# Optimization experiments

Measured on AMD Instinct MI355X. Metric: run time of the kernel, lower is better.

The kernel has to match this reference:

```python
import jax, jax.numpy as jnp
import numpy as np
import math

L, D, H, HD, F, G, V, P = 15, 512, 64, 8, 2048, 128, 7, 49
B, N = 4, 256


def setup_inputs() -> dict:
    key = jax.random.key(0)
    ks = jax.random.split(key, 24)
    nrm = lambda k, shape, s=0.02: (jax.random.normal(k, shape) * s).astype(jnp.float32)
    inp = {}
    inp["atom_types"] = jax.random.randint(ks[0], (B, N), 0, V)
    inp["coords"] = jax.random.normal(ks[1], (B, N, 3)) * 3.0
    inp["pair_types"] = jax.random.randint(ks[2], (B, N, N), 0, P)
    inp["mask"] = jnp.ones((B, N), dtype=bool)
    # embeddings / pair encoding params
    inp["atom_emb"] = nrm(ks[3], (V, D), 1.0).at[0].set(0.0)  # padding_idx=0
    inp["gaussian_mu"] = jax.random.normal(ks[4], (G,))
    inp["gaussian_sigma"] = jnp.ones((G,)) * 0.1
    inp["pair_a"] = jax.random.normal(ks[5], (P,)) * 0.01
    inp["pair_b"] = jax.random.normal(ks[6], (P,)) * 0.01
    inp["pl_w"] = nrm(ks[7], (G,))
    inp["pl_b"] = jnp.zeros(())
    # stacked per-layer params (leading dim L for lax.scan)
    inp["ln1_g"] = jnp.ones((L, D)); inp["ln1_b"] = jnp.zeros((L, D))
    inp["qkv_w"] = nrm(ks[8], (L, 3 * D, D)); inp["qkv_b"] = jnp.zeros((L, 3 * D))
    inp["pp_w"] = nrm(ks[9], (L, H), 0.1); inp["pp_b"] = jnp.zeros((L, H))
    inp["out_w"] = nrm(ks[10], (L, D, D)); inp["out_b"] = jnp.zeros((L, D))
    inp["ln2_g"] = jnp.ones((L, D)); inp["ln2_b"] = jnp.zeros((L, D))
    inp["ffn_w1"] = nrm(ks[11], (L, F, D)); inp["ffn_b1"] = jnp.zeros((L, F))
    inp["ffn_w2"] = nrm(ks[12], (L, D, F)); inp["ffn_b2"] = jnp.zeros((L, D))
    # SE3 head scalar affines (Linear(1,1) twice) and energy head
    inp["se3_uw"] = jnp.array(0.5); inp["se3_ub"] = jnp.array(0.01)
    inp["se3_ww"] = jnp.array(0.5); inp["se3_wb"] = jnp.array(0.01)
    inp["en_w"] = nrm(ks[13], (D,)); inp["en_b"] = jnp.zeros(())
    return inp


def _layernorm(x, g, b):
    m = x.mean(-1, keepdims=True)
    v = ((x - m) ** 2).mean(-1, keepdims=True)
    return (x - m) / jnp.sqrt(v + 1e-5) * g + b


def reference(atom_types, coords, pair_types, mask,
              atom_emb, gaussian_mu, gaussian_sigma, pair_a, pair_b, pl_w, pl_b,
              ln1_g, ln1_b, qkv_w, qkv_b, pp_w, pp_b, out_w, out_b,
              ln2_g, ln2_b, ffn_w1, ffn_b1, ffn_w2, ffn_b2,
              se3_uw, se3_ub, se3_ww, se3_wb, en_w, en_b):
    b_, n_ = atom_types.shape
    h = atom_emb[atom_types]  # [B,N,D]

    delta = coords[:, :, None, :] - coords[:, None, :, :]  # [B,N,N,3]
    d2 = (delta ** 2).sum(-1)
    dist = jnp.sqrt(jnp.maximum(d2, 1e-12))  # safe norm (grad-safe at 0)
    dist = jnp.where(mask[:, :, None], dist, 0.0)
    da = (pair_a[pair_types] * dist + pair_b[pair_types])[..., None]  # [B,N,N,1]
    gt = jnp.exp(-(da - gaussian_mu) ** 2) / (2.0 * gaussian_sigma ** 2)
    gt = gt / (gaussian_sigma * math.sqrt(2.0 * math.pi))
    gt = gt * mask[:, :, None, None]  # [B,N,N,G]
    pair_repr = gt @ pl_w + pl_b  # [B,N,N]
    pair_mask = mask[:, :, None] & mask[:, None, :]
    pair_repr = pair_repr * pair_mask

    scale = 1.0 / math.sqrt(HD)
    row_mask = mask[:, None, :, None]  # masks query rows, per original code

    def layer(hc, p):
        (l1g, l1b, qw, qb, ppw, ppb, ow, ob, l2g, l2b, w1, b1, w2, b2) = p
        x = _layernorm(hc, l1g, l1b)
        qkv = (x @ qw.T + qb).reshape(b_, n_, 3, H, HD)
        q, k, v = qkv[:, :, 0], qkv[:, :, 1], qkv[:, :, 2]
        scores = jnp.einsum('bnhd,bmhd->bhnm', q, k) * scale
        bias = pair_repr[..., None] * ppw + ppb  # [B,N,N,H]
        scores = scores + bias.transpose(0, 3, 1, 2)
        scores = jnp.where(row_mask, scores, -1e9)
        probs = jax.nn.softmax(scores, axis=-1)
        probs = jnp.where(jnp.isnan(probs), 0.0, probs)
        attn = jnp.einsum('bhnm,bmhd->bnhd', probs, v).reshape(b_, n_, D)
        hc = hc + attn @ ow.T + ob
        x2 = _layernorm(hc, l2g, l2b)
        ffn = jax.nn.gelu(x2 @ w1.T + b1, approximate=False) @ w2.T + b2
        return hc + ffn, None

    h, _ = jax.lax.scan(layer, h, (ln1_g, ln1_b, qkv_w, qkv_b, pp_w, pp_b,
                                   out_w, out_b, ln2_g, ln2_b,
                                   ffn_w1, ffn_b1, ffn_w2, ffn_b2))

    # --- SE3 equivariant head ---
    c = jax.nn.relu(pair_repr)[..., None]  # [B,N,N,1]
    c = c * se3_uw + se3_ub
    c = c * se3_ww + se3_wb
    c = c * mask[:, :, None, None]
    update = (delta * c).sum(axis=2)  # [B,N,3]
    num_valid = mask.sum(-1).astype(coords.dtype)[:, None, None] + 1e-6
    pred_coords = coords + update / num_valid

    cls = h[:, 0, :]
    pred_energy = cls @ en_w + en_b  # [B]
    return pred_coords, pred_energy


if __name__ == '__main__':
    out = reference(**setup_inputs())
    print(out[0].shape, out[1].shape)
```

## Files before the change

### kernel.cpp

```cpp
#include <hip/hip_runtime.h>
#include <hip/hip_bf16.h>
#include <math.h>

#define LAY 15
#define DIM 512
#define NH 64
#define HD 8
#define FF 2048
#define NG 128
#define BATCH 4
#define NTOK 256
#define PSTRIDE 524288

typedef __attribute__((ext_vector_type(8))) short short8;
typedef __attribute__((ext_vector_type(4))) short short4v;
typedef __attribute__((ext_vector_type(2))) short short2v;
typedef __attribute__((ext_vector_type(8))) __bf16 bf16x8;
typedef __attribute__((ext_vector_type(4))) float f32x4;

__device__ inline short f2bs(float f) {
  __bf16 b = (__bf16)f;
  return __builtin_bit_cast(short, b);
}

__global__ __launch_bounds__(256) void embed_kernel(
    const int* __restrict__ types, const float* __restrict__ emb,
    float* __restrict__ h)
{
  int idx = blockIdx.x * 256 + threadIdx.x;
  int token = idx >> 9;
  int d = idx & 511;
  h[idx] = emb[types[token] * DIM + d];
}

__global__ __launch_bounds__(256) void cvt_kernel(
    const float* __restrict__ qkvw, const float* __restrict__ outw,
    const float* __restrict__ w1, const float* __restrict__ w2,
    short* __restrict__ dst)
{
  int i = blockIdx.x * 256 + threadIdx.x;
  const float* src; int off;
  if (i < 2949120)      { src = qkvw; off = i; }
  else if (i < 3932160) { src = outw; off = i - 2949120; }
  else if (i < 7864320) { src = w1;   off = i - 3932160; }
  else                  { src = w2;   off = i - 7864320; }
  float4 f = ((const float4*)src)[off];
  short4v o;
  o[0] = f2bs(f.x); o[1] = f2bs(f.y); o[2] = f2bs(f.z); o[3] = f2bs(f.w);
  *(short4v*)(dst + (size_t)i * 4) = o;
}

__global__ __launch_bounds__(256) void pair_kernel(
    const int* __restrict__ pair_types, const float* __restrict__ coords,
    const float* __restrict__ mu, const float* __restrict__ sigma,
    const float* __restrict__ pa, const float* __restrict__ pb,
    const float* __restrict__ plw, const float* __restrict__ plb,
    const float* __restrict__ uw, const float* __restrict__ ub,
    const float* __restrict__ ww, const float* __restrict__ wb,
    float* __restrict__ pair_repr, float* __restrict__ out)
{
  __shared__ float smu[NG], sw[NG];
  __shared__ float sm[4][3];
  int tid = threadIdx.x;
  if (tid < NG) {
    float sg = sigma[tid];
    smu[tid] = mu[tid];
    sw[tid] = plw[tid] / (2.0f * sg * sg * sg * 2.5066282746310002f);
  }
  __syncthreads();
  int bi = blockIdx.x;
  int b = bi >> 8;
  int j = tid;
  int idx = bi * 256 + j;
  const float* ci = coords + bi * 3;
  const float* cj = coords + (b * NTOK + j) * 3;
  float dx = ci[0] - cj[0], dy = ci[1] - cj[1], dz = ci[2] - cj[2];
  float d2 = dx * dx + dy * dy + dz * dz;
  float dist = sqrtf(fmaxf(d2, 1e-12f));
  int pt = pair_types[idx];
  float da = pa[pt] * dist + pb[pt];
  float acc = 0.0f;
#pragma unroll 8
  for (int g = 0; g < NG; ++g) {
    float t = da - smu[g];
    acc += __expf(-t * t) * sw[g];
  }
  float pr = acc + plb[0];
  pair_repr[idx] = pr;

  float c = fmaxf(pr, 0.0f);
  c = c * uw[0] + ub[0];
  c = c * ww[0] + wb[0];
  float sx = dx * c, sy = dy * c, sz = dz * c;
#pragma unroll
  for (int o = 32; o > 0; o >>= 1) {
    sx += __shfl_xor(sx, o);
    sy += __shfl_xor(sy, o);
    sz += __shfl_xor(sz, o);
  }
  if ((j & 63) == 0) {
    sm[j >> 6][0] = sx; sm[j >> 6][1] = sy; sm[j >> 6][2] = sz;
  }
  __syncthreads();
  if (j < 3) {
    float u = sm[0][j] + sm[1][j] + sm[2][j] + sm[3][j];
    out[bi * 3 + j] = coords[bi * 3 + j] + u * (1.0f / (256.0f + 1e-6f));
  }
}

__global__ __launch_bounds__(256) void pairT_kernel(
    const float* __restrict__ pr, float* __restrict__ prT)
{
  __shared__ float tile[32][33];
  int b = blockIdx.z;
  int i0 = blockIdx.y * 32, j0 = blockIdx.x * 32;
  int tx = threadIdx.x & 31, ty = threadIdx.x >> 5;
#pragma unroll
  for (int r = 0; r < 4; ++r)
    tile[ty + r * 8][tx] = pr[((size_t)(b * NTOK + i0 + ty + r * 8)) * NTOK + j0 + tx];
  __syncthreads();
#pragma unroll
  for (int r = 0; r < 4; ++r)
    prT[((size_t)(b * NTOK + j0 + ty + r * 8)) * NTOK + i0 + tx] = tile[tx][ty + r * 8];
}

__global__ __launch_bounds__(256) void ln_kernel(
    const float* __restrict__ h, const float* __restrict__ g,
    const float* __restrict__ beta, short* __restrict__ x)
{
  int t = blockIdx.x;
  int tid = threadIdx.x;
  float2 v = *(const float2*)&h[(size_t)t * DIM + tid * 2];
  __shared__ float sm[4];
  float s = v.x + v.y;
#pragma unroll
  for (int o = 32; o > 0; o >>= 1) s += __shfl_xor(s, o);
  if ((tid & 63) == 0) sm[tid >> 6] = s;
  __syncthreads();
  float mean = (sm[0] + sm[1] + sm[2] + sm[3]) * (1.0f / 512.0f);
  float d0 = v.x - mean, d1 = v.y - mean;
  float ss = d0 * d0 + d1 * d1;
#pragma unroll
  for (int o = 32; o > 0; o >>= 1) ss += __shfl_xor(ss, o);
  __syncthreads();
  if ((tid & 63) == 0) sm[tid >> 6] = ss;
  __syncthreads();
  float var = (sm[0] + sm[1] + sm[2] + sm[3]) * (1.0f / 512.0f);
  float rstd = rsqrtf(var + 1e-5f);
  float2 gg = *(const float2*)&g[tid * 2];
  float2 bb = *(const float2*)&beta[tid * 2];
  short2v o2;
  o2[0] = f2bs(d0 * rstd * gg.x + bb.x);
  o2[1] = f2bs(d1 * rstd * gg.y + bb.y);
  *(short2v*)&x[(size_t)t * DIM + tid * 2] = o2;
}

__global__ __launch_bounds__(256) void ln_res_kernel(
    float* __restrict__ h, const float* __restrict__ part, int kparts,
    const float* __restrict__ g, const float* __restrict__ beta,
    short* __restrict__ x)
{
  int t = blockIdx.x;
  int tid = threadIdx.x;
  size_t base = (size_t)t * DIM + tid * 2;
  float2 v = *(const float2*)&h[base];
  for (int z = 0; z < kparts; ++z) {
    float2 pz = *(const float2*)&part[(size_t)z * PSTRIDE + base];
    v.x += pz.x; v.y += pz.y;
  }
  *(float2*)&h[base] = v;
  __shared__ float sm[4];
  float s = v.x + v.y;
#pragma unroll
  for (int o = 32; o > 0; o >>= 1) s += __shfl_xor(s, o);
  if ((tid & 63) == 0) sm[tid >> 6] = s;
  __syncthreads();
  float mean = (sm[0] + sm[1] + sm[2] + sm[3]) * (1.0f / 512.0f);
  float d0 = v.x - mean, d1 = v.y - mean;
  float ss = d0 * d0 + d1 * d1;
#pragma unroll
  for (int o = 32; o > 0; o >>= 1) ss += __shfl_xor(ss, o);
  __syncthreads();
  if ((tid & 63) == 0) sm[tid >> 6] = ss;
  __syncthreads();
  float var = (sm[0] + sm[1] + sm[2] + sm[3]) * (1.0f / 512.0f);
  float rstd = rsqrtf(var + 1e-5f);
  float2 gg = *(const float2*)&g[tid * 2];
  float2 bb = *(const float2*)&beta[tid * 2];
  short2v o2;
  o2[0] = f2bs(d0 * rstd * gg.x + bb.x);
  o2[1] = f2bs(d1 * rstd * gg.y + bb.y);
  *(short2v*)&x[base] = o2;
}

template <int MODE, int TSTEPS>
__global__ __launch_bounds__(64) void mm3(
    const short* __restrict__ A, const short* __restrict__ W,
    const float* __restrict__ bias, float* __restrict__ Cf,
    short* __restrict__ Cb, int N, int K)
{
  __shared__ alignas(16) short As[3][2048];
  __shared__ alignas(16) short Bs[3][2048];
  int tid = threadIdx.x;
  int fr = tid & 15, fq = (tid >> 4) & 3;
  int m0 = blockIdx.y * 32, n0 = blockIdx.x * 32;
  int kbeg = blockIdx.z * (TSTEPS * 64);

  auto stage = [&](int p, int k0) {
#pragma unroll
    for (int r = 0; r < 4; ++r) {
      int id = r * 64 + tid;
      int row = id >> 3;
      int col = (id & 7) ^ (row & 7);
      const short* ga = &A[(size_t)(m0 + row) * K + k0 + col * 8];
      __builtin_amdgcn_global_load_lds(
          (const __attribute__((address_space(1))) void*)ga,
          (__attribute__((address_space(3))) void*)&As[p][r * 512],
          16, 0, 0);
    }
#pragma unroll
    for (int r = 0; r < 4; ++r) {
      int id = r * 64 + tid;
      int row = id >> 3;
      int col = (id & 7) ^ (row & 7);
      const short* gw = &W[(size_t)(n0 + row) * K + k0 + col * 8];
      __builtin_amdgcn_global_load_lds(
          (const __attribute__((address_space(1))) void*)gw,
          (__attribute__((address_space(3))) void*)&Bs[p][r * 512],
          16, 0, 0);
    }
  };

  f32x4 acc[2][2];
#pragma unroll
  for (int i = 0; i < 2; ++i)
#pragma unroll
    for (int j = 0; j < 2; ++j) acc[i][j] = (f32x4){0.f, 0.f, 0.f, 0.f};

  int aslot[2][2], bslot[2][2];
#pragma unroll
  for (int s = 0; s < 2; ++s) {
    int c = s * 4 + fq;
#pragma unroll
    for (int i = 0; i < 2; ++i) {
      int m = i * 16 + fr;
      aslot[s][i] = m * 8 + (c ^ (m & 7));
      bslot[s][i] = m * 8 + (c ^ (m & 7));
    }
  }

  stage(0, kbeg);
  stage(1, kbeg + 64);
  stage(2, kbeg + 128);

#pragma unroll
  for (int t = 0; t < TSTEPS; ++t) {
    if (t < TSTEPS - 2)       asm volatile("s_waitcnt vmcnt(16)" ::: "memory");
    else if (t == TSTEPS - 2) asm volatile("s_waitcnt vmcnt(8)" ::: "memory");
    else                      asm volatile("s_waitcnt vmcnt(0)" ::: "memory");
    int p = t % 3;
    short8 af[2][2], bf_[2][2];
#pragma unroll
    for (int s = 0; s < 2; ++s)
#pragma unroll
      for (int i = 0; i < 2; ++i) {
        af[s][i]  = *(const short8*)&As[p][aslot[s][i] * 8];
        bf_[s][i] = *(const short8*)&Bs[p][bslot[s][i] * 8];
      }
    asm volatile("s_waitcnt lgkmcnt(0)" ::: "memory");
    __builtin_amdgcn_sched_barrier(0);
    if (t + 3 < TSTEPS) stage(p, kbeg + (t + 3) * 64);
#pragma unroll
    for (int s = 0; s < 2; ++s)
#pragma unroll
      for (int i = 0; i < 2; ++i)
#pragma unroll
        for (int j = 0; j < 2; ++j)
          acc[i][j] = __builtin_amdgcn_mfma_f32_16x16x32_bf16(
              af[s][i], bf_[s][j], acc[i][j], 0, 0, 0);
  }

#pragma unroll
  for (int i = 0; i < 2; ++i) {
#pragma unroll
    for (int j = 0; j < 2; ++j) {
      int col = n0 + j * 16 + fr;
      float bcol = bias[col];
#pragma unroll
      for (int rr = 0; rr < 4; ++rr) {
        int row = m0 + i * 16 + fq * 4 + rr;
        size_t idx = (size_t)row * N + col;
        float v = acc[i][j][rr];
        if (MODE == 2) {
          v += bcol;
          Cb[idx] = f2bs(0.5f * v * (1.0f + erff(v * 0.70710678118654752f)));
        } else if (MODE == 3) {
          Cb[idx] = f2bs(v + bcol);
        } else {
          if (blockIdx.z == 0) v += bcol;
          Cf[(size_t)blockIdx.z * PSTRIDE + idx] = v;
        }
      }
    }
  }
}

__global__ __launch_bounds__(128) void attn_mfma(
    const short* __restrict__ qkv, const float* __restrict__ prT,
    const float* __restrict__ ppw, const float* __restrict__ ppb,
    short* __restrict__ attn)
{
  __shared__ alignas(16) short Kl[256 * 8];
  __shared__ alignas(16) short Ql[128 * 8];
  __shared__ alignas(16) short VT[8 * 264];
  __shared__ alignas(16) short P[2 * 16 * 264];
  __shared__ alignas(16) float linv[32];
  int h = blockIdx.x, b = blockIdx.y;
  int qbase = blockIdx.z * 128;
  int tid = threadIdx.x;

#pragma unroll
  for (int r0 = 0; r0 < 2; ++r0) {
    int r = tid + r0 * 128;
    short8 kv = *(const short8*)&qkv[(size_t)(b * NTOK + r) * 1536 + 512 + h * 8];
    *(short8*)&Kl[r * 8] = kv;
    short8 vv = *(const short8*)&qkv[(size_t)(b * NTOK + r) * 1536 + 1024 + h * 8];
#pragma unroll
    for (int d = 0; d < 8; ++d) VT[d * 264 + r] = vv[d];
  }
  {
    short8 qv = *(const short8*)&qkv[(size_t)(b * NTOK + qbase + tid) * 1536 + h * 8];
    *(short8*)&Ql[tid * 8] = qv;
  }
  __syncthreads();

  int lane = tid & 63, w = tid >> 6;
  int fr = lane & 15, quad = lane >> 4;
  float pw = ppw[h], pbb = ppb[h];
  const float scale = 0.35355339059327373f;
  short8 zero8 = {0, 0, 0, 0, 0, 0, 0, 0};

  short8 vfrag[8];
#pragma unroll
  for (int kc = 0; kc < 8; ++kc)
    vfrag[kc] = (fr < 8) ? *(const short8*)&VT[fr * 264 + kc * 32 + quad * 8]
                         : zero8;

  short* Pw = &P[w * 16 * 264];
  float* lw = &linv[w * 16];

  for (int qt = 0; qt < 4; ++qt) {
    int qloc = w * 64 + qt * 16;
    int qg = qbase + qloc + fr;
    const float* prp = &prT[(size_t)b * 65536 + qg];
    float prv[16][4];
#pragma unroll
    for (int t = 0; t < 16; ++t)
#pragma unroll
      for (int r = 0; r < 4; ++r)
        prv[t][r] = prp[(size_t)(t * 16 + quad * 4 + r) * NTOK];

    short8 qf = zero8;
    if (quad == 0) qf = *(const short8*)&Ql[(qloc + fr) * 8];
    f32x4 sacc[16];
#pragma unroll
    for (int t = 0; t < 16; ++t) {
      short8 kf = zero8;
      if (quad == 0) kf = *(const short8*)&Kl[(t * 16 + fr) * 8];
      sacc[t] = __builtin_amdgcn_mfma_f32_16x16x32_bf16(
          kf, qf, (f32x4){0.f, 0.f, 0.f, 0.f}, 0, 0, 0);
    }

    float l = 0.f;
#pragma unroll
    for (int t = 0; t < 16; ++t) {
      short4v pk;
#pragma unroll
      for (int r = 0; r < 4; ++r) {
        float s = sacc[t][r] * scale + prv[t][r] * pw + pbb;
        float p = __expf(s);
        l += p;
        pk[r] = f2bs(p);
      }
      *(short4v*)&Pw[fr * 264 + t * 16 + quad * 4] = pk;
    }
    l += __shfl_xor(l, 16);
    l += __shfl_xor(l, 32);
    if (lane < 16) lw[fr] = 1.0f / l;

    f32x4 oacc = (f32x4){0.f, 0.f, 0.f, 0.f};
#pragma unroll
    for (int kc = 0; kc < 8; ++kc) {
      short8 pf = *(const short8*)&Pw[fr * 264 + kc * 32 + quad * 8];
      oacc = __builtin_amdgcn_mfma_f32_16x16x32_bf16(pf, vfrag[kc], oacc, 0, 0, 0);
    }
    if (fr < 8) {
      f32x4 li = *(f32x4*)&lw[quad * 4];
#pragma unroll
      for (int r = 0; r < 4; ++r) {
        int q = qbase + qloc + quad * 4 + r;
        attn[(size_t)(b * NTOK + q) * DIM + h * 8 + fr] = f2bs(oacc[r] * li[r]);
      }
    }
  }
}

__global__ __launch_bounds__(256) void energy_kernel(
    const float* __restrict__ h, const float* __restrict__ part,
    const float* __restrict__ enw, const float* __restrict__ enb,
    float* __restrict__ out)
{
  int b = blockIdx.x;
  int tid = threadIdx.x;
  size_t base = (size_t)(b * NTOK) * DIM;
  float x0 = h[base + tid], x1 = h[base + tid + 256];
#pragma unroll
  for (int z = 0; z < 4; ++z) {
    x0 += part[(size_t)z * PSTRIDE + base + tid];
    x1 += part[(size_t)z * PSTRIDE + base + tid + 256];
  }
  float s = x0 * enw[tid] + x1 * enw[tid + 256];
  __shared__ float sm[4];
#pragma unroll
  for (int o = 32; o > 0; o >>= 1) s += __shfl_xor(s, o);
  if ((tid & 63) == 0) sm[tid >> 6] = s;
  __syncthreads();
  if (tid == 0) out[BATCH * NTOK * 3 + b] = sm[0] + sm[1] + sm[2] + sm[3] + enb[0];
}

extern "C" void kernel_launch(void* const* d_in, const int* in_sizes, int n_in,
                              void* d_out, int out_size, void* d_ws, size_t ws_size,
                              hipStream_t stream)
{
  const int*   atom_types = (const int*)d_in[0];
  const float* coords     = (const float*)d_in[1];
  const int*   pair_types = (const int*)d_in[2];
  const float* atom_emb = (const float*)d_in[4];
  const float* gmu  = (const float*)d_in[5];
  const float* gsig = (const float*)d_in[6];
  const float* pa   = (const float*)d_in[7];
  const float* pb   = (const float*)d_in[8];
  const float* plw  = (const float*)d_in[9];
  const float* plb  = (const float*)d_in[10];
  const float* ln1g = (const float*)d_in[11];
  const float* ln1b = (const float*)d_in[12];
  const float* qkvw = (const float*)d_in[13];
  const float* qkvb = (const float*)d_in[14];
  const float* ppw  = (const float*)d_in[15];
  const float* ppb  = (const float*)d_in[16];
  const float* outw = (const float*)d_in[17];
  const float* outb = (const float*)d_in[18];
  const float* ln2g = (const float*)d_in[19];
  const float* ln2b = (const float*)d_in[20];
  const float* w1   = (const float*)d_in[21];
  const float* b1   = (const float*)d_in[22];
  const float* w2   = (const float*)d_in[23];
  const float* b2   = (const float*)d_in[24];
  const float* uw   = (const float*)d_in[25];
  const float* ub   = (const float*)d_in[26];
  const float* sww  = (const float*)d_in[27];
  const float* swb  = (const float*)d_in[28];
  const float* enw  = (const float*)d_in[29];
  const float* enb  = (const float*)d_in[30];

  float* out = (float*)d_out;
  float* ws  = (float*)d_ws;
  float* pair_repr = ws;
  float* prT  = pair_repr + 262144;
  float* h    = prT + 262144;
  float* part = h + 524288;
  short* qkv_bf  = (short*)(part + 4 * 524288);
  short* x_bf    = qkv_bf + 1572864;
  short* attn_bf = x_bf + 524288;
  short* ffn1_bf = attn_bf + 524288;
  short* qkvw_bf = ffn1_bf + 2097152;
  short* outw_bf = qkvw_bf + 11796480;
  short* w1_bf   = outw_bf + 3932160;
  short* w2_bf   = w1_bf + 15728640;

  cvt_kernel<<<46080, 256, 0, stream>>>(qkvw, outw, w1, w2, qkvw_bf);

  embed_kernel<<<2048, 256, 0, stream>>>(atom_types, atom_emb, h);
  pair_kernel<<<1024, 256, 0, stream>>>(pair_types, coords, gmu, gsig, pa, pb,
                                        plw, plb, uw, ub, sww, swb,
                                        pair_repr, out);
  pairT_kernel<<<dim3(8, 8, 4), 256, 0, stream>>>(pair_repr, prT);

  for (int l = 0; l < LAY; ++l) {
    if (l == 0)
      ln_kernel<<<1024, 256, 0, stream>>>(h, ln1g, ln1b, x_bf);
    else
      ln_res_kernel<<<1024, 256, 0, stream>>>(h, part, 4,
                                              ln1g + l * DIM, ln1b + l * DIM, x_bf);
    mm3<3, 8><<<dim3(48, 32, 1), 64, 0, stream>>>(
        x_bf, qkvw_bf + (size_t)l * 1536 * DIM, qkvb + l * 1536, nullptr, qkv_bf,
        1536, DIM);
    attn_mfma<<<dim3(NH, BATCH, 2), 128, 0, stream>>>(
        qkv_bf, prT, ppw + l * NH, ppb + l * NH, attn_bf);
    mm3<4, 4><<<dim3(16, 32, 2), 64, 0, stream>>>(
        attn_bf, outw_bf + (size_t)l * DIM * DIM, outb + l * DIM, part, nullptr,
        DIM, DIM);
    ln_res_kernel<<<1024, 256, 0, stream>>>(h, part, 2,
                                            ln2g + l * DIM, ln2b + l * DIM, x_bf);
    mm3<2, 8><<<dim3(64, 32, 1), 64, 0, stream>>>(
        x_bf, w1_bf + (size_t)l * FF * DIM, b1 + l * FF, nullptr, ffn1_bf,
        FF, DIM);
    mm3<4, 8><<<dim3(16, 32, 4), 64, 0, stream>>>(
        ffn1_bf, w2_bf + (size_t)l * DIM * FF, b2 + l * DIM, part, nullptr,
        DIM, FF);
  }
  energy_kernel<<<BATCH, 256, 0, stream>>>(h, part, enw, enb, out);
}
```

Before: 1.142 ms.

## Widen GEMM tiles to 32x64, halve FFN2 split-K, batch weight conversion loads

The mm3 GEMM kernel now computes 32x64 output tiles instead of 32x32, so each A tile staged in LDS is reused across twice as many columns. Grid sizes are halved to match, and the vmcnt waits are updated for the extra B loads. The FFN2 GEMM drops from split-K 4 to split-K 2 with 16 K-steps per block, so downstream residual/LN and energy kernels sum only 2 partial buffers. The weight-conversion kernel now issues four nontemporal loads per thread before converting. The trade-off is fewer blocks in flight (occupancy/parallelism) and more registers and LDS per block, in exchange for less redundant A traffic and fewer partial sums.

```diff
diff --git a/kernel.cpp b/kernel.cpp
--- a/kernel.cpp
+++ b/kernel.cpp
@@ -38,16 +38,27 @@
     const float* __restrict__ w1, const float* __restrict__ w2,
     short* __restrict__ dst)
 {
-  int i = blockIdx.x * 256 + threadIdx.x;
-  const float* src; int off;
-  if (i < 2949120)      { src = qkvw; off = i; }
-  else if (i < 3932160) { src = outw; off = i - 2949120; }
-  else if (i < 7864320) { src = w1;   off = i - 3932160; }
-  else                  { src = w2;   off = i - 7864320; }
-  float4 f = ((const float4*)src)[off];
-  short4v o;
-  o[0] = f2bs(f.x); o[1] = f2bs(f.y); o[2] = f2bs(f.z); o[3] = f2bs(f.w);
-  *(short4v*)(dst + (size_t)i * 4) = o;
+  const int G = 2949120;
+  int t0 = blockIdx.x * 256 + threadIdx.x;
+  f32x4 f[4];
+#pragma unroll
+  for (int r = 0; r < 4; ++r) {
+    int i = t0 + r * G;
+    const float* src; int off;
+    if (i < 2949120)      { src = qkvw; off = i; }
+    else if (i < 3932160) { src = outw; off = i - 2949120; }
+    else if (i < 7864320) { src = w1;   off = i - 3932160; }
+    else                  { src = w2;   off = i - 7864320; }
+    f[r] = __builtin_nontemporal_load((const f32x4*)src + off);
+  }
+#pragma unroll
+  for (int r = 0; r < 4; ++r) {
+    int i = t0 + r * G;
+    short4v o;
+    o[0] = f2bs(f[r][0]); o[1] = f2bs(f[r][1]);
+    o[2] = f2bs(f[r][2]); o[3] = f2bs(f[r][3]);
+    *(short4v*)(dst + (size_t)i * 4) = o;
+  }
 }
 
 __global__ __launch_bounds__(256) void pair_kernel(
@@ -200,10 +211,10 @@
     short* __restrict__ Cb, int N, int K)
 {
   __shared__ alignas(16) short As[3][2048];
-  __shared__ alignas(16) short Bs[3][2048];
+  __shared__ alignas(16) short Bs[3][4096];
   int tid = threadIdx.x;
   int fr = tid & 15, fq = (tid >> 4) & 3;
-  int m0 = blockIdx.y * 32, n0 = blockIdx.x * 32;
+  int m0 = blockIdx.y * 32, n0 = blockIdx.x * 64;
   int kbeg = blockIdx.z * (TSTEPS * 64);
 
   auto stage = [&](int p, int k0) {
@@ -219,7 +230,7 @@
           16, 0, 0);
     }
 #pragma unroll
-    for (int r = 0; r < 4; ++r) {
+    for (int r = 0; r < 8; ++r) {
       int id = r * 64 + tid;
       int row = id >> 3;
       int col = (id & 7) ^ (row & 7);
@@ -231,13 +242,13 @@
     }
   };
 
-  f32x4 acc[2][2];
+  f32x4 acc[2][4];
 #pragma unroll
   for (int i = 0; i < 2; ++i)
 #pragma unroll
-    for (int j = 0; j < 2; ++j) acc[i][j] = (f32x4){0.f, 0.f, 0.f, 0.f};
-
-  int aslot[2][2], bslot[2][2];
+    for (int j = 0; j < 4; ++j) acc[i][j] = (f32x4){0.f, 0.f, 0.f, 0.f};
+
+  int aslot[2][2], bslot[2][4];
 #pragma unroll
   for (int s = 0; s < 2; ++s) {
     int c = s * 4 + fq;
@@ -245,7 +256,11 @@
     for (int i = 0; i < 2; ++i) {
       int m = i * 16 + fr;
       aslot[s][i] = m * 8 + (c ^ (m & 7));
-      bslot[s][i] = m * 8 + (c ^ (m & 7));
+    }
+#pragma unroll
+    for (int j = 0; j < 4; ++j) {
+      int n = j * 16 + fr;
+      bslot[s][j] = n * 8 + (c ^ (n & 7));
     }
   }
 
@@ -255,18 +270,20 @@
 
 #pragma unroll
   for (int t = 0; t < TSTEPS; ++t) {
-    if (t < TSTEPS - 2)       asm volatile("s_waitcnt vmcnt(16)" ::: "memory");
-    else if (t == TSTEPS - 2) asm volatile("s_waitcnt vmcnt(8)" ::: "memory");
+    if (t < TSTEPS - 2)       asm volatile("s_waitcnt vmcnt(24)" ::: "memory");
+    else if (t == TSTEPS - 2) asm volatile("s_waitcnt vmcnt(12)" ::: "memory");
     else                      asm volatile("s_waitcnt vmcnt(0)" ::: "memory");
     int p = t % 3;
-    short8 af[2][2], bf_[2][2];
-#pragma unroll
-    for (int s = 0; s < 2; ++s)
-#pragma unroll
-      for (int i = 0; i < 2; ++i) {
-        af[s][i]  = *(const short8*)&As[p][aslot[s][i] * 8];
-        bf_[s][i] = *(const short8*)&Bs[p][bslot[s][i] * 8];
-      }
+    short8 af[2][2], bf_[2][4];
+#pragma unroll
+    for (int s = 0; s < 2; ++s) {
+#pragma unroll
+      for (int i = 0; i < 2; ++i)
+        af[s][i] = *(const short8*)&As[p][aslot[s][i] * 8];
+#pragma unroll
+      for (int j = 0; j < 4; ++j)
+        bf_[s][j] = *(const short8*)&Bs[p][bslot[s][j] * 8];
+    }
     asm volatile("s_waitcnt lgkmcnt(0)" ::: "memory");
     __builtin_amdgcn_sched_barrier(0);
     if (t + 3 < TSTEPS) stage(p, kbeg + (t + 3) * 64);
@@ -275,7 +292,7 @@
 #pragma unroll
       for (int i = 0; i < 2; ++i)
 #pragma unroll
-        for (int j = 0; j < 2; ++j)
+        for (int j = 0; j < 4; ++j)
           acc[i][j] = __builtin_amdgcn_mfma_f32_16x16x32_bf16(
               af[s][i], bf_[s][j], acc[i][j], 0, 0, 0);
   }
@@ -283,7 +300,7 @@
 #pragma unroll
   for (int i = 0; i < 2; ++i) {
 #pragma unroll
-    for (int j = 0; j < 2; ++j) {
+    for (int j = 0; j < 4; ++j) {
       int col = n0 + j * 16 + fr;
       float bcol = bias[col];
 #pragma unroll
@@ -415,7 +432,7 @@
   size_t base = (size_t)(b * NTOK) * DIM;
   float x0 = h[base + tid], x1 = h[base + tid + 256];
 #pragma unroll
-  for (int z = 0; z < 4; ++z) {
+  for (int z = 0; z < 2; ++z) {
     x0 += part[(size_t)z * PSTRIDE + base + tid];
     x1 += part[(size_t)z * PSTRIDE + base + tid + 256];
   }
@@ -478,7 +495,7 @@
   short* w1_bf   = outw_bf + 3932160;
   short* w2_bf   = w1_bf + 15728640;
 
-  cvt_kernel<<<46080, 256, 0, stream>>>(qkvw, outw, w1, w2, qkvw_bf);
+  cvt_kernel<<<11520, 256, 0, stream>>>(qkvw, outw, w1, w2, qkvw_bf);
 
   embed_kernel<<<2048, 256, 0, stream>>>(atom_types, atom_emb, h);
   pair_kernel<<<1024, 256, 0, stream>>>(pair_types, coords, gmu, gsig, pa, pb,
@@ -490,22 +507,22 @@
     if (l == 0)
       ln_kernel<<<1024, 256, 0, stream>>>(h, ln1g, ln1b, x_bf);
     else
-      ln_res_kernel<<<1024, 256, 0, stream>>>(h, part, 4,
+      ln_res_kernel<<<1024, 256, 0, stream>>>(h, part, 2,
                                               ln1g + l * DIM, ln1b + l * DIM, x_bf);
-    mm3<3, 8><<<dim3(48, 32, 1), 64, 0, stream>>>(
+    mm3<3, 8><<<dim3(24, 32, 1), 64, 0, stream>>>(
         x_bf, qkvw_bf + (size_t)l * 1536 * DIM, qkvb + l * 1536, nullptr, qkv_bf,
         1536, DIM);
     attn_mfma<<<dim3(NH, BATCH, 2), 128, 0, stream>>>(
         qkv_bf, prT, ppw + l * NH, ppb + l * NH, attn_bf);
-    mm3<4, 4><<<dim3(16, 32, 2), 64, 0, stream>>>(
+    mm3<4, 4><<<dim3(8, 32, 2), 64, 0, stream>>>(
         attn_bf, outw_bf + (size_t)l * DIM * DIM, outb + l * DIM, part, nullptr,
         DIM, DIM);
     ln_res_kernel<<<1024, 256, 0, stream>>>(h, part, 2,
                                             ln2g + l * DIM, ln2b + l * DIM, x_bf);
-    mm3<2, 8><<<dim3(64, 32, 1), 64, 0, stream>>>(
+    mm3<2, 8><<<dim3(32, 32, 1), 64, 0, stream>>>(
         x_bf, w1_bf + (size_t)l * FF * DIM, b1 + l * FF, nullptr, ffn1_bf,
         FF, DIM);
-    mm3<4, 8><<<dim3(16, 32, 4), 64, 0, stream>>>(
+    mm3<4, 16><<<dim3(8, 32, 2), 64, 0, stream>>>(
         ffn1_bf, w2_bf + (size_t)l * DIM * FF, b2 + l * DIM, part, nullptr,
         DIM, FF);
   }
```

Result: faster. 1.113 ms (-2.6%).
